# Kernel optimization log

Measured on AMD Instinct MI355X. Metric: run time of the kernel, lower is better.

## Reference

```python
import jax, jax.numpy as jnp
import numpy as np

WIDTHS = [2, 3, 5, 8, 13, 21, 34, 55, 89, 26]  # ragged one-hot feature widths, sum = 256
NSEG = len(WIDTHS)
B, IN = 8192, 256
LAYOUT = [1024, 1024, 1024, 256]
EPS = 1e-5  # BatchNorm1d default eps
TAU = 1.0


def setup_inputs() -> dict:
    key = jax.random.key(0)
    ks = iter(jax.random.split(key, 64))
    inp = {"x": jax.random.normal(next(ks), (B, IN), jnp.float32)}
    prev = IN
    for i, fc in enumerate(LAYOUT):
        inp[f"W{i}"] = jax.random.normal(next(ks), (fc, prev), jnp.float32) / np.float32(np.sqrt(prev))
        inp[f"b{i}"] = 0.01 * jax.random.normal(next(ks), (fc,), jnp.float32)
        if i + 1 < len(LAYOUT):  # Residual blocks carry BatchNorm params (eval mode)
            inp[f"g{i}"] = 1.0 + 0.1 * jax.random.normal(next(ks), (fc,), jnp.float32)
            inp[f"be{i}"] = 0.1 * jax.random.normal(next(ks), (fc,), jnp.float32)
            inp[f"rm{i}"] = 0.1 * jax.random.normal(next(ks), (fc,), jnp.float32)
            inp[f"rv{i}"] = 0.75 + 0.5 * jax.random.uniform(next(ks), (fc,), dtype=jnp.float32)
        prev += fc
    inp["seg_ids"] = jnp.asarray(np.repeat(np.arange(NSEG), WIDTHS), jnp.int32)  # [256]
    return inp


def _residual(x, W, b, g, be, rm, rv):
    # Linear -> eval-mode BatchNorm1d -> ReLU -> concat([out, input])
    h = x @ W.T + b
    h = (h - rm) * (g * jax.lax.rsqrt(rv + EPS)) + be
    return jnp.concatenate([jax.nn.relu(h), x], axis=1)


def _segment_softmax(x, seg_ids):
    # Fused segmented softmax over ragged feature groups (replaces per-feature Python loop)
    xt = x.T / TAU                                            # [F, B]
    m = jax.ops.segment_max(xt, seg_ids, num_segments=NSEG)   # [NSEG, B]
    e = jnp.exp(xt - m[seg_ids])
    s = jax.ops.segment_sum(e, seg_ids, num_segments=NSEG)
    return (e / s[seg_ids]).T                                 # [B, F]


def reference(x, W0, b0, g0, be0, rm0, rv0, W1, b1, g1, be1, rm1, rv1,
              W2, b2, g2, be2, rm2, rv2, W3, b3, seg_ids):
    h = _residual(x, W0, b0, g0, be0, rm0, rv0)   # [B, 1280]
    h = _residual(h, W1, b1, g1, be1, rm1, rv1)   # [B, 2304]
    h = _residual(h, W2, b2, g2, be2, rm2, rv2)   # [B, 3328]
    h = h @ W3.T + b3                              # [B, 256]
    return _segment_softmax(h, seg_ids)
```

## Files before the change

### kernel.cpp

```cpp
#include <hip/hip_runtime.h>
#include <hip/hip_fp16.h>


#define LDH 3328
#define NROWS 8192

typedef _Float16 f16x8 __attribute__((ext_vector_type(8)));
typedef _Float16 f16x4 __attribute__((ext_vector_type(4)));
typedef float f32x4 __attribute__((ext_vector_type(4)));

__constant__ int c_bnd[11] = {0, 2, 5, 10, 18, 31, 52, 86, 141, 230, 256};

__device__ __forceinline__ void async_cp16(const _Float16* g, _Float16* l) {
  __builtin_amdgcn_global_load_lds(
      (__attribute__((address_space(1))) void*)g,
      (__attribute__((address_space(3))) void*)l, 16, 0, 0);
}

__device__ __forceinline__ _Float16 f2h(float f) { return (_Float16)f; }

__global__ void prep_kernel(const float* __restrict__ s0,
                            const float* __restrict__ s1,
                            const float* __restrict__ s2,
                            const float* __restrict__ s3,
                            const float* __restrict__ x,
                            const float* __restrict__ b3,
                            _Float16* __restrict__ d0,
                            _Float16* __restrict__ d1,
                            _Float16* __restrict__ d2,
                            _Float16* __restrict__ d3,
                            _Float16* __restrict__ H, float* __restrict__ out,
                            int n0, int n1, int n2, int n3, int n4, int n5) {
  int i = blockIdx.x * blockDim.x + threadIdx.x;
  if (i >= n5) return;
  if (i >= n4) {
    const int j = i - n4;
    const int c = (j & 63) * 4;
    *(float4*)&out[(size_t)j * 4] = *(const float4*)&b3[c];
    return;
  }
  if (i >= n3) {
    const int j = i - n3;
    const int row = j >> 6;
    const int c = (j & 63) * 4;
    const float4 v = *(const float4*)&x[(size_t)j * 4];
    f16x4 h = {f2h(v.x), f2h(v.y), f2h(v.z), f2h(v.w)};
    *(f16x4*)&H[(size_t)row * LDH + 3072 + c] = h;
    return;
  }
  const float* s;
  _Float16* d;
  if (i < n0) {
    s = s0; d = d0;
  } else if (i < n1) {
    s = s1 - (size_t)n0 * 4; d = d1 - (size_t)n0 * 4;
  } else if (i < n2) {
    s = s2 - (size_t)n1 * 4; d = d2 - (size_t)n1 * 4;
  } else {
    s = s3 - (size_t)n2 * 4; d = d3 - (size_t)n2 * 4;
  }
  const float4 v = *(const float4*)&s[(size_t)i * 4];
  f16x4 h = {f2h(v.x), f2h(v.y), f2h(v.z), f2h(v.w)};
  *(f16x4*)&d[(size_t)i * 4] = h;
}

__launch_bounds__(256, 2) __global__
void gemm_bn_kernel(const _Float16* __restrict__ A, int K,
                    const _Float16* __restrict__ W,
                    const float* __restrict__ bias,
                    const float* __restrict__ g, const float* __restrict__ be,
                    const float* __restrict__ rm,
                    const float* __restrict__ rv, _Float16* __restrict__ outH,
                    int outOff) {
  __shared__ _Float16 Alds[128 * 128];
  __shared__ _Float16 Blds[128 * 128];

  const int tid = threadIdx.x;
  const int lane = tid & 63;
  const int wave = tid >> 6;
  const int wr = wave >> 1;
  const int wc = wave & 1;
  const int row0 = blockIdx.x * 128;
  const int col0 = blockIdx.y * 128;
  const int lr4 = lane >> 4;
  const int sl = lane & 15;
  const int fr = lane & 15;
  const int q = lane >> 4;

  f32x4 acc[4][4] = {};

  for (int k0 = 0; k0 < K; k0 += 128) {
    __syncthreads();
#pragma unroll
    for (int it = 0; it < 8; ++it) {
      const int j = it * 4 + wave;
      const int r = j * 4 + lr4;
      const int gc = sl ^ (r & 7);
      async_cp16(A + (size_t)(row0 + r) * LDH + k0 + gc * 8, &Alds[j * 512]);
      async_cp16(W + (size_t)(col0 + r) * K + k0 + gc * 8, &Blds[j * 512]);
    }
    __syncthreads();

#pragma unroll
    for (int kq = 0; kq < 4; ++kq) {
      f16x8 av[4], bv[4];
#pragma unroll
      for (int t = 0; t < 4; ++t) {
        const int ra = wr * 64 + t * 16 + fr;
        av[t] =
            *(const f16x8*)&Alds[ra * 128 + (((kq * 4 + q) ^ (ra & 7)) * 8)];
        const int rb = wc * 64 + t * 16 + fr;
        bv[t] =
            *(const f16x8*)&Blds[rb * 128 + (((kq * 4 + q) ^ (rb & 7)) * 8)];
      }
#pragma unroll
      for (int tm = 0; tm < 4; ++tm)
#pragma unroll
        for (int tn = 0; tn < 4; ++tn)
          acc[tm][tn] = __builtin_amdgcn_mfma_f32_16x16x32_f16(
              av[tm], bv[tn], acc[tm][tn], 0, 0, 0);
    }
  }

#pragma unroll
  for (int tn = 0; tn < 4; ++tn) {
    const int n = col0 + wc * 64 + tn * 16 + fr;
    const float alpha = g[n] * rsqrtf(rv[n] + 1e-5f);
    const float beta = (bias[n] - rm[n]) * alpha + be[n];
#pragma unroll
    for (int tm = 0; tm < 4; ++tm) {
      const int rbase = row0 + wr * 64 + tm * 16 + q * 4;
#pragma unroll
      for (int r = 0; r < 4; ++r) {
        float v = acc[tm][tn][r] * alpha + beta;
        v = fmaxf(v, 0.0f);
        outH[(size_t)(rbase + r) * LDH + outOff + n] = f2h(v);
      }
    }
  }
}

__launch_bounds__(256, 4) __global__
void gemm_out_split(const _Float16* __restrict__ A,
                    const _Float16* __restrict__ W, float* __restrict__ P) {
  __shared__ _Float16 Alds[128 * 64];
  __shared__ _Float16 Blds[128 * 64];

  const int tid = threadIdx.x;
  const int lane = tid & 63;
  const int wave = tid >> 6;
  const int wr = wave >> 1;
  const int wc = wave & 1;
  const int row0 = blockIdx.x * 128;
  const int cb = blockIdx.y & 1;
  const int ks = blockIdx.y >> 1;
  const int col0 = cb * 128;
  const int k0b = ks * 832;
  const int k0e = k0b + 832;
  const int lr = lane >> 3;
  const int ls = lane & 7;
  const int lc = ls ^ lr;
  const int fr = lane & 15;
  const int q = lane >> 4;
  const int K = 3328;

  f32x4 acc[4][4] = {};

  for (int k0 = k0b; k0 < k0e; k0 += 64) {
    __syncthreads();
#pragma unroll
    for (int it = 0; it < 4; ++it) {
      const int rl = it * 32 + wave * 8;
      async_cp16(A + (size_t)(row0 + rl + lr) * LDH + k0 + lc * 8,
                 &Alds[rl * 64]);
      async_cp16(W + (size_t)(col0 + rl + lr) * K + k0 + lc * 8,
                 &Blds[rl * 64]);
    }
    __syncthreads();

#pragma unroll
    for (int kq = 0; kq < 2; ++kq) {
      f16x8 av[4], bv[4];
#pragma unroll
      for (int t = 0; t < 4; ++t) {
        const int ra = wr * 64 + t * 16 + fr;
        av[t] = *(const f16x8*)&Alds[ra * 64 + (((q + 4 * kq) ^ (ra & 7)) * 8)];
        const int rb = wc * 64 + t * 16 + fr;
        bv[t] = *(const f16x8*)&Blds[rb * 64 + (((q + 4 * kq) ^ (rb & 7)) * 8)];
      }
#pragma unroll
      for (int tm = 0; tm < 4; ++tm)
#pragma unroll
        for (int tn = 0; tn < 4; ++tn)
          acc[tm][tn] = __builtin_amdgcn_mfma_f32_16x16x32_f16(
              av[tm], bv[tn], acc[tm][tn], 0, 0, 0);
    }
  }

  float* Pk = P + (size_t)ks * ((size_t)NROWS * 256);
#pragma unroll
  for (int tn = 0; tn < 4; ++tn) {
    const int n = col0 + wc * 64 + tn * 16 + fr;
#pragma unroll
    for (int tm = 0; tm < 4; ++tm) {
      const int rbase = row0 + wr * 64 + tm * 16 + q * 4;
#pragma unroll
      for (int r = 0; r < 4; ++r)
        Pk[(size_t)(rbase + r) * 256 + n] = acc[tm][tn][r];
    }
  }
}

__launch_bounds__(256, 4) __global__
void gemm_out_kernel(const _Float16* __restrict__ A,
                     const _Float16* __restrict__ W,
                     float* __restrict__ out) {
  __shared__ _Float16 Alds[128 * 64];
  __shared__ _Float16 Blds[128 * 64];

  const int tid = threadIdx.x;
  const int lane = tid & 63;
  const int wave = tid >> 6;
  const int wr = wave >> 1;
  const int wc = wave & 1;
  const int row0 = blockIdx.x * 128;
  const int cb = blockIdx.y & 1;
  const int ks = blockIdx.y >> 1;
  const int col0 = cb * 128;
  const int k0b = ks * 832;
  const int k0e = k0b + 832;
  const int lr = lane >> 3;
  const int ls = lane & 7;
  const int lc = ls ^ lr;
  const int fr = lane & 15;
  const int q = lane >> 4;
  const int K = 3328;

  f32x4 acc[4][4] = {};

  for (int k0 = k0b; k0 < k0e; k0 += 64) {
    __syncthreads();
#pragma unroll
    for (int it = 0; it < 4; ++it) {
      const int rl = it * 32 + wave * 8;
      async_cp16(A + (size_t)(row0 + rl + lr) * LDH + k0 + lc * 8,
                 &Alds[rl * 64]);
      async_cp16(W + (size_t)(col0 + rl + lr) * K + k0 + lc * 8,
                 &Blds[rl * 64]);
    }
    __syncthreads();

#pragma unroll
    for (int kq = 0; kq < 2; ++kq) {
      f16x8 av[4], bv[4];
#pragma unroll
      for (int t = 0; t < 4; ++t) {
        const int ra = wr * 64 + t * 16 + fr;
        av[t] = *(const f16x8*)&Alds[ra * 64 + (((q + 4 * kq) ^ (ra & 7)) * 8)];
        const int rb = wc * 64 + t * 16 + fr;
        bv[t] = *(const f16x8*)&Blds[rb * 64 + (((q + 4 * kq) ^ (rb & 7)) * 8)];
      }
#pragma unroll
      for (int tm = 0; tm < 4; ++tm)
#pragma unroll
        for (int tn = 0; tn < 4; ++tn)
          acc[tm][tn] = __builtin_amdgcn_mfma_f32_16x16x32_f16(
              av[tm], bv[tn], acc[tm][tn], 0, 0, 0);
    }
  }

#pragma unroll
  for (int tn = 0; tn < 4; ++tn) {
    const int n = col0 + wc * 64 + tn * 16 + fr;
#pragma unroll
    for (int tm = 0; tm < 4; ++tm) {
      const int rbase = row0 + wr * 64 + tm * 16 + q * 4;
#pragma unroll
      for (int r = 0; r < 4; ++r)
        atomicAdd(&out[(size_t)(rbase + r) * 256 + n], acc[tm][tn][r]);
    }
  }
}

__global__ void segsoftmax_kernel(float* __restrict__ out,
                                  const int* __restrict__ segids) {
  __shared__ float vals[4][256];
  __shared__ float red[4][10];
  const int w = threadIdx.x >> 6;
  const int l = threadIdx.x & 63;
  const int row = blockIdx.x * 4 + w;
  float4 v = *(float4*)&out[(size_t)row * 256 + l * 4];
  *(float4*)&vals[w][l * 4] = v;
  __syncthreads();
  if (l < 10) {
    float m = -1e30f;
    for (int j = c_bnd[l]; j < c_bnd[l + 1]; ++j) m = fmaxf(m, vals[w][j]);
    red[w][l] = m;
  }
  __syncthreads();
  const int4 s4 = *(const int4*)&segids[l * 4];
  float4 e;
  e.x = expf(v.x - red[w][s4.x]);
  e.y = expf(v.y - red[w][s4.y]);
  e.z = expf(v.z - red[w][s4.z]);
  e.w = expf(v.w - red[w][s4.w]);
  *(float4*)&vals[w][l * 4] = e;
  __syncthreads();
  if (l < 10) {
    float s = 0.0f;
    for (int j = c_bnd[l]; j < c_bnd[l + 1]; ++j) s += vals[w][j];
    red[w][l] = s;
  }
  __syncthreads();
  float4 o;
  o.x = e.x / red[w][s4.x];
  o.y = e.y / red[w][s4.y];
  o.z = e.z / red[w][s4.z];
  o.w = e.w / red[w][s4.w];
  *(float4*)&out[(size_t)row * 256 + l * 4] = o;
}

__global__ void segsoftmax_sum_kernel(const float* __restrict__ P,
                                      const float* __restrict__ b3,
                                      float* __restrict__ out,
                                      const int* __restrict__ segids) {
  __shared__ float vals[4][256];
  __shared__ float red[4][10];
  const int w = threadIdx.x >> 6;
  const int l = threadIdx.x & 63;
  const int row = blockIdx.x * 4 + w;
  const size_t base = (size_t)row * 256 + l * 4;
  float4 v = *(const float4*)&P[base];
  const float4 v1 = *(const float4*)&P[base + (size_t)1 * NROWS * 256];
  const float4 v2 = *(const float4*)&P[base + (size_t)2 * NROWS * 256];
  const float4 v3 = *(const float4*)&P[base + (size_t)3 * NROWS * 256];
  const float4 b = *(const float4*)&b3[l * 4];
  v.x += v1.x + v2.x + v3.x + b.x;
  v.y += v1.y + v2.y + v3.y + b.y;
  v.z += v1.z + v2.z + v3.z + b.z;
  v.w += v1.w + v2.w + v3.w + b.w;
  *(float4*)&vals[w][l * 4] = v;
  __syncthreads();
  if (l < 10) {
    float m = -1e30f;
    for (int j = c_bnd[l]; j < c_bnd[l + 1]; ++j) m = fmaxf(m, vals[w][j]);
    red[w][l] = m;
  }
  __syncthreads();
  const int4 s4 = *(const int4*)&segids[l * 4];
  float4 e;
  e.x = expf(v.x - red[w][s4.x]);
  e.y = expf(v.y - red[w][s4.y]);
  e.z = expf(v.z - red[w][s4.z]);
  e.w = expf(v.w - red[w][s4.w]);
  *(float4*)&vals[w][l * 4] = e;
  __syncthreads();
  if (l < 10) {
    float s = 0.0f;
    for (int j = c_bnd[l]; j < c_bnd[l + 1]; ++j) s += vals[w][j];
    red[w][l] = s;
  }
  __syncthreads();
  float4 o;
  o.x = e.x / red[w][s4.x];
  o.y = e.y / red[w][s4.y];
  o.z = e.z / red[w][s4.z];
  o.w = e.w / red[w][s4.w];
  *(float4*)&out[(size_t)row * 256 + l * 4] = o;
}

extern "C" void kernel_launch(void* const* d_in, const int* in_sizes, int n_in,
                              void* d_out, int out_size, void* d_ws,
                              size_t ws_size, hipStream_t stream) {
  const float* x = (const float*)d_in[0];
  const float* W0 = (const float*)d_in[1];
  const float* b0 = (const float*)d_in[2];
  const float* g0 = (const float*)d_in[3];
  const float* be0 = (const float*)d_in[4];
  const float* rm0 = (const float*)d_in[5];
  const float* rv0 = (const float*)d_in[6];
  const float* W1 = (const float*)d_in[7];
  const float* b1 = (const float*)d_in[8];
  const float* g1 = (const float*)d_in[9];
  const float* be1 = (const float*)d_in[10];
  const float* rm1 = (const float*)d_in[11];
  const float* rv1 = (const float*)d_in[12];
  const float* W2 = (const float*)d_in[13];
  const float* b2 = (const float*)d_in[14];
  const float* g2 = (const float*)d_in[15];
  const float* be2 = (const float*)d_in[16];
  const float* rm2 = (const float*)d_in[17];
  const float* rv2 = (const float*)d_in[18];
  const float* W3 = (const float*)d_in[19];
  const float* b3 = (const float*)d_in[20];
  const int* seg = (const int*)d_in[21];
  float* out = (float*)d_out;

  _Float16* H = (_Float16*)d_ws;
  size_t off = (size_t)NROWS * LDH;
  _Float16* Wh0 = H + off; off += 1024 * 256;
  _Float16* Wh1 = H + off; off += 1024 * 1280;
  _Float16* Wh2 = H + off; off += 1024 * 2304;
  _Float16* Wh3 = H + off; off += 256 * 3328;
  float* P = (float*)(H + off);
  const size_t need = off * 2 + (size_t)4 * NROWS * 256 * 4;
  const bool partials = ws_size >= need;

  const int n0 = 65536, n1 = n0 + 327680, n2 = n1 + 589824, n3 = n2 + 212992;
  const int n4 = n3 + 524288, n5 = n4 + 524288;
  const int nprep = partials ? n4 : n5;
  prep_kernel<<<(nprep + 255) / 256, 256, 0, stream>>>(
      W0, W1, W2, W3, x, b3, Wh0, Wh1, Wh2, Wh3, H, out, n0, n1, n2, n3, n4,
      nprep);

  dim3 blk(256);
  gemm_bn_kernel<<<dim3(64, 8), blk, 0, stream>>>(
      H + 3072, 256, Wh0, b0, g0, be0, rm0, rv0, H, 2048);
  gemm_bn_kernel<<<dim3(64, 8), blk, 0, stream>>>(
      H + 2048, 1280, Wh1, b1, g1, be1, rm1, rv1, H, 1024);
  gemm_bn_kernel<<<dim3(64, 8), blk, 0, stream>>>(
      H + 1024, 2304, Wh2, b2, g2, be2, rm2, rv2, H, 0);
  if (partials) {
    gemm_out_split<<<dim3(64, 8), blk, 0, stream>>>(H, Wh3, P);
    segsoftmax_sum_kernel<<<2048, 256, 0, stream>>>(P, b3, out, seg);
  } else {
    gemm_out_kernel<<<dim3(64, 8), blk, 0, stream>>>(H, Wh3, out);
    segsoftmax_kernel<<<2048, 256, 0, stream>>>(out, seg);
  }
}
```

Baseline: 229.3 us.

## Overlap weight fp16 conversion with preceding GEMM via extra grid row

The up-front prep kernel now converts only W0, x and the output bias init. Each later weight matrix (W1, W2, W3) is converted to fp16 by an extra row of 64 blocks (blockIdx.y == 8) added to the preceding gemm_bn launch. The aim is to shorten the serial prep stage by hiding weight conversion behind GEMM compute. The cost is that those conversion blocks compete for CUs and bandwidth with the GEMM tiles, and the extra grid row can add scheduling tail.

New measurement: 243.4 us. 1.06x slower.

```diff
diff --git a/kernel.cpp b/kernel.cpp
--- a/kernel.cpp
+++ b/kernel.cpp
@@ -19,28 +19,22 @@
 
 __device__ __forceinline__ _Float16 f2h(float f) { return (_Float16)f; }
 
-__global__ void prep_kernel(const float* __restrict__ s0,
-                            const float* __restrict__ s1,
-                            const float* __restrict__ s2,
-                            const float* __restrict__ s3,
+__global__ void prep_kernel(const float* __restrict__ w0,
                             const float* __restrict__ x,
                             const float* __restrict__ b3,
                             _Float16* __restrict__ d0,
-                            _Float16* __restrict__ d1,
-                            _Float16* __restrict__ d2,
-                            _Float16* __restrict__ d3,
                             _Float16* __restrict__ H, float* __restrict__ out,
-                            int n0, int n1, int n2, int n3, int n4, int n5) {
+                            int n0, int n1, int n2) {
   int i = blockIdx.x * blockDim.x + threadIdx.x;
-  if (i >= n5) return;
-  if (i >= n4) {
-    const int j = i - n4;
+  if (i >= n2) return;
+  if (i >= n1) {
+    const int j = i - n1;
     const int c = (j & 63) * 4;
     *(float4*)&out[(size_t)j * 4] = *(const float4*)&b3[c];
     return;
   }
-  if (i >= n3) {
-    const int j = i - n3;
+  if (i >= n0) {
+    const int j = i - n0;
     const int row = j >> 6;
     const int c = (j & 63) * 4;
     const float4 v = *(const float4*)&x[(size_t)j * 4];
@@ -48,20 +42,9 @@
     *(f16x4*)&H[(size_t)row * LDH + 3072 + c] = h;
     return;
   }
-  const float* s;
-  _Float16* d;
-  if (i < n0) {
-    s = s0; d = d0;
-  } else if (i < n1) {
-    s = s1 - (size_t)n0 * 4; d = d1 - (size_t)n0 * 4;
-  } else if (i < n2) {
-    s = s2 - (size_t)n1 * 4; d = d2 - (size_t)n1 * 4;
-  } else {
-    s = s3 - (size_t)n2 * 4; d = d3 - (size_t)n2 * 4;
-  }
-  const float4 v = *(const float4*)&s[(size_t)i * 4];
+  const float4 v = *(const float4*)&w0[(size_t)i * 4];
   f16x4 h = {f2h(v.x), f2h(v.y), f2h(v.z), f2h(v.w)};
-  *(f16x4*)&d[(size_t)i * 4] = h;
+  *(f16x4*)&d0[(size_t)i * 4] = h;
 }
 
 __launch_bounds__(256, 2) __global__
@@ -71,9 +54,20 @@
                     const float* __restrict__ g, const float* __restrict__ be,
                     const float* __restrict__ rm,
                     const float* __restrict__ rv, _Float16* __restrict__ outH,
-                    int outOff) {
+                    int outOff, const float* __restrict__ cvt_src,
+                    _Float16* __restrict__ cvt_dst, int cvt_nf4) {
   __shared__ _Float16 Alds[128 * 128];
   __shared__ _Float16 Blds[128 * 128];
+
+  if (blockIdx.y == 8) {
+    const int stride = 64 * 256;
+    for (int i = blockIdx.x * 256 + threadIdx.x; i < cvt_nf4; i += stride) {
+      const float4 v = *(const float4*)&cvt_src[(size_t)i * 4];
+      f16x4 h = {f2h(v.x), f2h(v.y), f2h(v.z), f2h(v.w)};
+      *(f16x4*)&cvt_dst[(size_t)i * 4] = h;
+    }
+    return;
+  }
 
   const int tid = threadIdx.x;
   const int lane = tid & 63;
@@ -406,20 +400,21 @@
   const size_t need = off * 2 + (size_t)4 * NROWS * 256 * 4;
   const bool partials = ws_size >= need;
 
-  const int n0 = 65536, n1 = n0 + 327680, n2 = n1 + 589824, n3 = n2 + 212992;
-  const int n4 = n3 + 524288, n5 = n4 + 524288;
-  const int nprep = partials ? n4 : n5;
-  prep_kernel<<<(nprep + 255) / 256, 256, 0, stream>>>(
-      W0, W1, W2, W3, x, b3, Wh0, Wh1, Wh2, Wh3, H, out, n0, n1, n2, n3, n4,
-      nprep);
+  const int n0 = 65536, n1 = n0 + 524288, n2 = n1 + 524288;
+  const int nprep = partials ? n1 : n2;
+  prep_kernel<<<(nprep + 255) / 256, 256, 0, stream>>>(W0, x, b3, Wh0, H, out,
+                                                       n0, n1, nprep);
 
   dim3 blk(256);
-  gemm_bn_kernel<<<dim3(64, 8), blk, 0, stream>>>(
-      H + 3072, 256, Wh0, b0, g0, be0, rm0, rv0, H, 2048);
-  gemm_bn_kernel<<<dim3(64, 8), blk, 0, stream>>>(
-      H + 2048, 1280, Wh1, b1, g1, be1, rm1, rv1, H, 1024);
-  gemm_bn_kernel<<<dim3(64, 8), blk, 0, stream>>>(
-      H + 1024, 2304, Wh2, b2, g2, be2, rm2, rv2, H, 0);
+  gemm_bn_kernel<<<dim3(64, 9), blk, 0, stream>>>(
+      H + 3072, 256, Wh0, b0, g0, be0, rm0, rv0, H, 2048,
+      W1, Wh1, 1024 * 1280 / 4);
+  gemm_bn_kernel<<<dim3(64, 9), blk, 0, stream>>>(
+      H + 2048, 1280, Wh1, b1, g1, be1, rm1, rv1, H, 1024,
+      W2, Wh2, 1024 * 2304 / 4);
+  gemm_bn_kernel<<<dim3(64, 9), blk, 0, stream>>>(
+      H + 1024, 2304, Wh2, b2, g2, be2, rm2, rv2, H, 0,
+      W3, Wh3, 256 * 3328 / 4);
   if (partials) {
     gemm_out_split<<<dim3(64, 8), blk, 0, stream>>>(H, Wh3, P);
     segsoftmax_sum_kernel<<<2048, 256, 0, stream>>>(P, b3, out, seg);
```
